# Kernel optimization log

Measured on AMD Instinct MI355X. Metric: run time of the kernel, lower is better.

## Reference

```python
import jax, jax.numpy as jnp
from jax import lax
import numpy as np

EPS = 1e-5
NEG_SLOPE = 0.2

# 4D conv via lax.conv_general_dilated (supports arbitrary spatial rank)
_DN = ('NCABXY', 'OIABXY', 'NCABXY')  # N,C + 4 spatial dims

def conv4d(x, w):
    # x: (N, Cin, S1, S2, H, W); w: (Cout, Cin, 3, 3, 3, 3); padding=1, stride=1
    return lax.conv_general_dilated(
        x, w,
        window_strides=(1, 1, 1, 1),
        padding=[(1, 1)] * 4,
        dimension_numbers=_DN,
    )

def instance_norm4d(x):
    # normalize per (n, c) over all 4 spatial dims; no affine (PyTorch default)
    mean = jnp.mean(x, axis=(2, 3, 4, 5), keepdims=True)
    var = jnp.var(x, axis=(2, 3, 4, 5), keepdims=True)
    return (x - mean) * lax.rsqrt(var + EPS)

def leaky_relu(x):
    return jnp.where(x >= 0, x, NEG_SLOPE * x)

def setup_inputs() -> dict:
    key = jax.random.key(0)
    k0, k1, k2 = jax.random.split(key, 3)
    image = jax.random.normal(k0, (1, 16, 8, 16, 64, 64), dtype=jnp.float32)
    # He-ish init scale for kernel 3^4
    w1 = jax.random.normal(k1, (32, 16, 3, 3, 3, 3), dtype=jnp.float32) * 0.03
    w2 = jax.random.normal(k2, (32, 32, 3, 3, 3, 3), dtype=jnp.float32) * 0.02
    return {"image": image, "w1": w1, "w2": w2}

def reference(image, w1, w2):
    x = leaky_relu(instance_norm4d(conv4d(image, w1)))
    x = leaky_relu(instance_norm4d(conv4d(x, w2)))
    return x
```

## Files before the change

### kernel.cpp

```cpp
#include <hip/hip_runtime.h>

#define D1 8
#define D2 16
#define HH 64
#define WW 64
#define SPATIAL (D1*D2*HH*WW)
#define EPS 1e-5f
#define NEG 0.2f

typedef unsigned short u16;
typedef __attribute__((ext_vector_type(8))) short s16x8;
typedef __attribute__((ext_vector_type(8))) unsigned short u16x8;
typedef __attribute__((ext_vector_type(4))) unsigned short u16x4;
typedef __attribute__((ext_vector_type(4))) float f32x4;

__device__ __forceinline__ u16 f2bf(float f) {
    unsigned int u = __builtin_bit_cast(unsigned int, f);
    return (u16)((u + 0x7FFFu + ((u >> 16) & 1u)) >> 16);
}
__device__ __forceinline__ float bf2f(u16 u) {
    unsigned int v = ((unsigned int)u) << 16;
    return __builtin_bit_cast(float, v);
}
__device__ __forceinline__ float leaky(float x) {
    return x >= 0.f ? x : NEG * x;
}

__device__ __forceinline__ void decode_block(int flat, int& a, int& b, int& h0) {
    int xcd  = flat & 7;
    int slot = flat >> 3;
    int ht   = slot & 7;
    int b0   = (slot >> 3) & 1;
    a        = (slot >> 4) & 7;
    b        = xcd * 2 + b0;
    h0       = ht * 8;
}

__global__ __launch_bounds__(256) void wtrans1(const float* __restrict__ w,
                                               u16* __restrict__ o) {
    int i = blockIdx.x * 256 + threadIdx.x;
    if (i >= 55296) return;
    int k    = i & 31;
    int co   = (i >> 5) & 31;
    int grp  = (i >> 10) & 1;
    int rest = i >> 11;
    int dh   = rest % 3;
    int p    = rest / 3;
    int da = p / 3, db = p % 3;
    float v = 0.f;
    if (grp == 0) {
        int dw = k >> 4, ci = k & 15;
        v = w[((((co * 16 + ci) * 3 + da) * 3 + db) * 3 + dh) * 3 + dw];
    } else if (k < 16) {
        v = w[((((co * 16 + k) * 3 + da) * 3 + db) * 3 + dh) * 3 + 2];
    }
    o[i] = f2bf(v);
}

__global__ __launch_bounds__(256) void wtrans2(const float* __restrict__ w,
                                               u16* __restrict__ o) {
    int i = blockIdx.x * 256 + threadIdx.x;
    if (i >= 82944) return;
    int ci = i & 31;
    int co = (i >> 5) & 31;
    int t  = (i >> 10) % 9;
    int p  = (i >> 10) / 9;
    int da = p / 3, db = p % 3, dh = t / 3, dw = t % 3;
    o[i] = f2bf(w[((((co * 32 + ci) * 3 + da) * 3 + db) * 3 + dh) * 3 + dw]);
}

__global__ __launch_bounds__(256) void imgtrans(const float* __restrict__ img,
                                                u16* __restrict__ o) {
    int p = blockIdx.x * 256 + threadIdx.x;
    u16 r[16];
    #pragma unroll
    for (int c = 0; c < 16; ++c)
        r[c] = f2bf(img[(size_t)c * SPATIAL + p]);
    u16x8 lo, hi;
    #pragma unroll
    for (int j = 0; j < 8; ++j) { lo[j] = r[j]; hi[j] = r[8 + j]; }
    u16x8* dst = (u16x8*)(o + (size_t)p * 16);
    dst[0] = lo;
    dst[1] = hi;
}

__global__ __launch_bounds__(256, 2)
void conv1_mfma(const u16* __restrict__ xT, const u16* __restrict__ w1t,
                u16* __restrict__ y1, float* __restrict__ st1)
{
    __shared__ __align__(16) u16 lds[660 * 24];
    __shared__ float sred[64];

    const int tid = threadIdx.x;
    int a, b, h0;
    decode_block(blockIdx.x, a, b, h0);
    const int lane = tid & 63;
    const int wv   = tid >> 6;
    const int kq   = lane >> 4;
    const int m    = lane & 15;
    const int wseg = wv << 4;

    unsigned pm = 0;
    #pragma unroll
    for (int p = 0; p < 9; ++p) {
        int ap = a + p / 3 - 1, bp = b + p % 3 - 1;
        if (ap >= 0 && ap < D1 && bp >= 0 && bp < D2) pm |= 1u << p;
    }

    const int p0 = tid >> 1, g = tid & 1;
    unsigned vmask = 0;
    int goff[6];
    #pragma unroll
    for (int k = 0; k < 6; ++k) {
        int pos = p0 + 128 * k;
        int row = pos / 66, col = pos - row * 66;
        int h = h0 - 1 + row, w = col - 1;
        bool v = (pos < 660) && col >= 1 && col <= 64 && h >= 0 && h < HH;
        goff[k] = v ? (h * WW + w) * 16 + g * 8 : 0;
        vmask |= (unsigned)v << k;
    }
    const int lbase = p0 * 24 + g * 8;

    for (int e = tid; e < 660; e += 256) {
        int row = e / 66, col = e - row * 66;
        int h = h0 - 1 + row;
        if (col == 0 || col == 65 || h < 0 || h >= HH) {
            u16x8 z = (u16x8)0;
            *(u16x8*)&lds[e * 24]     = z;
            *(u16x8*)&lds[e * 24 + 8] = z;
        }
    }

    f32x4 acc[8][2];
    #pragma unroll
    for (int i = 0; i < 8; ++i)
        #pragma unroll
        for (int nt = 0; nt < 2; ++nt)
            acc[i][nt] = (f32x4)0.f;

    int p = 0;
    while (!((pm >> p) & 1)) ++p;

    u16x8 pf[6];
    {
        int ap = a + p / 3 - 1, bp = b + p % 3 - 1;
        const u16* src = xT + (size_t)(ap * D2 + bp) * (HH * WW * 16);
        #pragma unroll
        for (int k = 0; k < 6; ++k)
            if ((vmask >> k) & 1) pf[k] = *(const u16x8*)(src + goff[k]);
    }

    while (p < 9) {
        int pn = p + 1;
        while (pn < 9 && !((pm >> pn) & 1)) ++pn;

        #pragma unroll
        for (int k = 0; k < 6; ++k)
            if ((vmask >> k) & 1) *(u16x8*)&lds[lbase + k * 3072] = pf[k];
        __syncthreads();

        if (pn < 9) {
            int ap = a + pn / 3 - 1, bp = b + pn % 3 - 1;
            const u16* src = xT + (size_t)(ap * D2 + bp) * (HH * WW * 16);
            #pragma unroll
            for (int k = 0; k < 6; ++k)
                if ((vmask >> k) & 1) pf[k] = *(const u16x8*)(src + goff[k]);
        }

        const u16* wbase = w1t + p * 6144;
        #pragma unroll
        for (int grp = 0; grp < 2; ++grp) {
            s16x8 bf[3][2];
            #pragma unroll
            for (int dh = 0; dh < 3; ++dh) {
                const u16* wb = wbase + (dh * 2 + grp) * 1024;
                bf[dh][0] = *(const s16x8*)(wb + m * 32 + kq * 8);
                bf[dh][1] = *(const s16x8*)(wb + (m + 16) * 32 + kq * 8);
            }
            const int cshift = (grp == 0) ? (kq >> 1) : 2;
            const int ebase  = (kq & 1) * 8;
            #pragma unroll
            for (int x = 0; x < 10; ++x) {
                int pos = x * 66 + wseg + m + cshift;
                s16x8 af = *(const s16x8*)&lds[pos * 24 + ebase];
                #pragma unroll
                for (int dh = 0; dh < 3; ++dh) {
                    int i = x - dh;
                    if (i >= 0 && i < 8) {
                        acc[i][0] = __builtin_amdgcn_mfma_f32_16x16x32_bf16(af, bf[dh][0], acc[i][0], 0, 0, 0);
                        acc[i][1] = __builtin_amdgcn_mfma_f32_16x16x32_bf16(af, bf[dh][1], acc[i][1], 0, 0, 0);
                    }
                }
            }
        }
        __syncthreads();
        p = pn;
    }

    if (tid < 64) sred[tid] = 0.f;
    __syncthreads();

    float s[2] = {0.f, 0.f}, s2[2] = {0.f, 0.f};
    const size_t plane_out = (size_t)(a * D2 + b) * (HH * WW);
    #pragma unroll
    for (int i = 0; i < 8; ++i) {
        int h  = h0 + i;
        int w0 = wseg + kq * 4;
        #pragma unroll
        for (int nt = 0; nt < 2; ++nt) {
            int co = m + nt * 16;
            #pragma unroll
            for (int reg = 0; reg < 4; ++reg) {
                float v = acc[i][nt][reg];
                s[nt]  += v;
                s2[nt] += v * v;
                y1[(plane_out + h * WW + (w0 + reg)) * 32 + co] = f2bf(v);
            }
        }
    }
    #pragma unroll
    for (int nt = 0; nt < 2; ++nt) {
        s[nt]  += __shfl_xor(s[nt], 16);  s[nt]  += __shfl_xor(s[nt], 32);
        s2[nt] += __shfl_xor(s2[nt], 16); s2[nt] += __shfl_xor(s2[nt], 32);
    }
    if (kq == 0) {
        atomicAdd(&sred[m * 2],            s[0]);
        atomicAdd(&sred[m * 2 + 1],        s2[0]);
        atomicAdd(&sred[(m + 16) * 2],     s[1]);
        atomicAdd(&sred[(m + 16) * 2 + 1], s2[1]);
    }
    __syncthreads();
    if (tid < 64) atomicAdd(&st1[tid], sred[tid]);
}

__global__ __launch_bounds__(256)
void norm1_kernel(u16* __restrict__ y1, const float* __restrict__ st1)
{
    const int tid = threadIdx.x;
    const int q   = tid & 3;
    const float invN = 1.f / (float)SPATIAL;
    float mean[8], scl[8];
    #pragma unroll
    for (int j = 0; j < 8; ++j) {
        int ci  = q * 8 + j;
        float mu = st1[ci * 2] * invN;
        float va = st1[ci * 2 + 1] * invN - mu * mu;
        mean[j] = mu;
        scl[j]  = rsqrtf(va + EPS);
    }
    #pragma unroll
    for (int j4 = 0; j4 < 4; ++j4) {
        size_t gidx = (size_t)blockIdx.x * 1024 + j4 * 256 + tid;
        u16x8* ptr = (u16x8*)(y1 + gidx * 8);
        u16x8 v = *ptr;
        u16x8 o;
        #pragma unroll
        for (int j = 0; j < 8; ++j)
            o[j] = f2bf(leaky((bf2f(v[j]) - mean[j]) * scl[j]));
        *ptr = o;
    }
}

__global__ __launch_bounds__(256, 2)
void conv2_mfma(const u16* __restrict__ y1, const u16* __restrict__ w2t,
                u16* __restrict__ y2, float* __restrict__ st2)
{
    __shared__ __align__(16) u16 lds[660 * 40];
    __shared__ float sred[64];

    const int tid = threadIdx.x;
    int a, b, h0;
    decode_block(blockIdx.x, a, b, h0);
    const int lane = tid & 63;
    const int wv   = tid >> 6;
    const int kq   = lane >> 4;
    const int m    = lane & 15;
    const int wseg = wv << 4;

    unsigned pm = 0;
    #pragma unroll
    for (int p = 0; p < 9; ++p) {
        int ap = a + p / 3 - 1, bp = b + p % 3 - 1;
        if (ap >= 0 && ap < D1 && bp >= 0 && bp < D2) pm |= 1u << p;
    }

    const int p0 = tid >> 2, q = tid & 3;
    unsigned vmask = 0;
    int goff[11];
    #pragma unroll
    for (int k = 0; k < 11; ++k) {
        int pos = p0 + 64 * k;
        int row = pos / 66, col = pos - row * 66;
        int h = h0 - 1 + row, w = col - 1;
        bool v = (pos < 660) && col >= 1 && col <= 64 && h >= 0 && h < HH;
        goff[k] = v ? (h * WW + w) * 32 + q * 8 : 0;
        vmask |= (unsigned)v << k;
    }
    const int lbase = p0 * 40 + q * 8;

    for (int e = tid; e < 660; e += 256) {
        int row = e / 66, col = e - row * 66;
        int h = h0 - 1 + row;
        if (col == 0 || col == 65 || h < 0 || h >= HH) {
            u16x8 z = (u16x8)0;
            #pragma unroll
            for (int gg = 0; gg < 4; ++gg)
                *(u16x8*)&lds[e * 40 + gg * 8] = z;
        }
    }

    f32x4 acc[8][2];
    #pragma unroll
    for (int i = 0; i < 8; ++i)
        #pragma unroll
        for (int nt = 0; nt < 2; ++nt)
            acc[i][nt] = (f32x4)0.f;

    int p = 0;
    while (!((pm >> p) & 1)) ++p;

    u16x8 pf[11];
    {
        int ap = a + p / 3 - 1, bp = b + p % 3 - 1;
        const u16* src = y1 + (size_t)(ap * D2 + bp) * (HH * WW * 32);
        #pragma unroll
        for (int k = 0; k < 11; ++k)
            if ((vmask >> k) & 1) pf[k] = *(const u16x8*)(src + goff[k]);
    }

    while (p < 9) {
        int pn = p + 1;
        while (pn < 9 && !((pm >> pn) & 1)) ++pn;

        #pragma unroll
        for (int k = 0; k < 11; ++k)
            if ((vmask >> k) & 1) *(u16x8*)&lds[lbase + k * 2560] = pf[k];
        __syncthreads();

        if (pn < 9) {
            int ap = a + pn / 3 - 1, bp = b + pn % 3 - 1;
            const u16* src = y1 + (size_t)(ap * D2 + bp) * (HH * WW * 32);
            #pragma unroll
            for (int k = 0; k < 11; ++k)
                if ((vmask >> k) & 1) pf[k] = *(const u16x8*)(src + goff[k]);
        }

        const u16* wbase = w2t + p * 9216;
        #pragma unroll
        for (int dw = 0; dw < 3; ++dw) {
            s16x8 bf[3][2];
            #pragma unroll
            for (int dh = 0; dh < 3; ++dh) {
                const u16* wb = wbase + (dh * 3 + dw) * 1024;
                bf[dh][0] = *(const s16x8*)(wb + m * 32 + kq * 8);
                bf[dh][1] = *(const s16x8*)(wb + (m + 16) * 32 + kq * 8);
            }
            #pragma unroll
            for (int x = 0; x < 10; ++x) {
                int pos = x * 66 + wseg + dw + m;
                s16x8 af = *(const s16x8*)&lds[pos * 40 + kq * 8];
                #pragma unroll
                for (int dh = 0; dh < 3; ++dh) {
                    int i = x - dh;
                    if (i >= 0 && i < 8) {
                        acc[i][0] = __builtin_amdgcn_mfma_f32_16x16x32_bf16(af, bf[dh][0], acc[i][0], 0, 0, 0);
                        acc[i][1] = __builtin_amdgcn_mfma_f32_16x16x32_bf16(af, bf[dh][1], acc[i][1], 0, 0, 0);
                    }
                }
            }
        }
        __syncthreads();
        p = pn;
    }

    if (tid < 64) sred[tid] = 0.f;
    __syncthreads();

    float s[2] = {0.f, 0.f}, s2[2] = {0.f, 0.f};
    #pragma unroll
    for (int i = 0; i < 8; ++i) {
        int h  = h0 + i;
        int w0 = wseg + kq * 4;
        #pragma unroll
        for (int nt = 0; nt < 2; ++nt) {
            int co = m + nt * 16;
            u16x4 pk;
            #pragma unroll
            for (int reg = 0; reg < 4; ++reg) {
                float v = acc[i][nt][reg];
                s[nt]  += v;
                s2[nt] += v * v;
                pk[reg] = f2bf(v);
            }
            size_t off = ((size_t)(co * D1 + a) * D2 + b) * (HH * WW) + h * WW + w0;
            *(u16x4*)(y2 + off) = pk;
        }
    }
    #pragma unroll
    for (int nt = 0; nt < 2; ++nt) {
        s[nt]  += __shfl_xor(s[nt], 16);  s[nt]  += __shfl_xor(s[nt], 32);
        s2[nt] += __shfl_xor(s2[nt], 16); s2[nt] += __shfl_xor(s2[nt], 32);
    }
    if (kq == 0) {
        atomicAdd(&sred[m * 2],            s[0]);
        atomicAdd(&sred[m * 2 + 1],        s2[0]);
        atomicAdd(&sred[(m + 16) * 2],     s[1]);
        atomicAdd(&sred[(m + 16) * 2 + 1], s2[1]);
    }
    __syncthreads();
    if (tid < 64) atomicAdd(&st2[tid], sred[tid]);
}

__global__ __launch_bounds__(256)
void norm2_kernel(const u16* __restrict__ y2, const float* __restrict__ st2,
                  float* __restrict__ out)
{
    size_t i4 = (size_t)blockIdx.x * 256 + threadIdx.x;
    int c = (int)(i4 >> 17);
    const float invN = 1.f / (float)SPATIAL;
    float mu = st2[c * 2] * invN;
    float va = st2[c * 2 + 1] * invN - mu * mu;
    float sc = rsqrtf(va + EPS);
    u16x4 v = *(const u16x4*)(y2 + i4 * 4);
    float4 o;
    o.x = leaky((bf2f(v[0]) - mu) * sc);
    o.y = leaky((bf2f(v[1]) - mu) * sc);
    o.z = leaky((bf2f(v[2]) - mu) * sc);
    o.w = leaky((bf2f(v[3]) - mu) * sc);
    *(float4*)(out + i4 * 4) = o;
}

extern "C" void kernel_launch(void* const* d_in, const int* in_sizes, int n_in,
                              void* d_out, int out_size, void* d_ws, size_t ws_size,
                              hipStream_t stream)
{
    const float* image = (const float*)d_in[0];
    const float* w1    = (const float*)d_in[1];
    const float* w2    = (const float*)d_in[2];
    float* out = (float*)d_out;

    u16*   imgT = (u16*)d_ws;
    u16*   y1   = (u16*)((char*)d_ws + 33554432);
    u16*   y2   = imgT;
    float* st   = (float*)((char*)d_ws + 67108864);
    float* st1  = st;
    float* st2  = st + 64;

    u16* w1t = (u16*)((char*)d_out + 66832384);
    u16* w2t = (u16*)((char*)d_out + 66942976);

    hipMemsetAsync(st, 0, 512, stream);
    wtrans1<<<216, 256, 0, stream>>>(w1, w1t);
    wtrans2<<<324, 256, 0, stream>>>(w2, w2t);
    imgtrans<<<2048, 256, 0, stream>>>(image, imgT);

    conv1_mfma<<<1024, 256, 0, stream>>>(imgT, w1t, y1, st1);
    norm1_kernel<<<2048, 256, 0, stream>>>(y1, st1);
    conv2_mfma<<<1024, 256, 0, stream>>>(y1, w2t, y2, st2);
    norm2_kernel<<<16384, 256, 0, stream>>>(y2, st2, out);
}
```

Before: 277.2 us.

## Merge prep kernels, spread next-plane prefetch loads, raise conv occupancy

Folds the memset, both weight transposes and the image transpose into a single prep kernel, saving three launches. Inside both conv kernels, the global prefetch of the next plane is split into chunks placed after each group of MFMA work instead of one burst, which should overlap loads with compute and lower peak register pressure. Launch bounds for both conv kernels go from 2 to 3 blocks per SM, which may force register spilling but allows more occupancy to hide latency.

```diff
diff --git a/kernel.cpp b/kernel.cpp
--- a/kernel.cpp
+++ b/kernel.cpp
@@ -36,55 +36,58 @@
     h0       = ht * 8;
 }
 
-__global__ __launch_bounds__(256) void wtrans1(const float* __restrict__ w,
-                                               u16* __restrict__ o) {
-    int i = blockIdx.x * 256 + threadIdx.x;
-    if (i >= 55296) return;
-    int k    = i & 31;
-    int co   = (i >> 5) & 31;
-    int grp  = (i >> 10) & 1;
-    int rest = i >> 11;
-    int dh   = rest % 3;
-    int p    = rest / 3;
-    int da = p / 3, db = p % 3;
-    float v = 0.f;
-    if (grp == 0) {
-        int dw = k >> 4, ci = k & 15;
-        v = w[((((co * 16 + ci) * 3 + da) * 3 + db) * 3 + dh) * 3 + dw];
-    } else if (k < 16) {
-        v = w[((((co * 16 + k) * 3 + da) * 3 + db) * 3 + dh) * 3 + 2];
-    }
-    o[i] = f2bf(v);
-}
-
-__global__ __launch_bounds__(256) void wtrans2(const float* __restrict__ w,
-                                               u16* __restrict__ o) {
-    int i = blockIdx.x * 256 + threadIdx.x;
-    if (i >= 82944) return;
-    int ci = i & 31;
-    int co = (i >> 5) & 31;
-    int t  = (i >> 10) % 9;
-    int p  = (i >> 10) / 9;
-    int da = p / 3, db = p % 3, dh = t / 3, dw = t % 3;
-    o[i] = f2bf(w[((((co * 32 + ci) * 3 + da) * 3 + db) * 3 + dh) * 3 + dw]);
-}
-
-__global__ __launch_bounds__(256) void imgtrans(const float* __restrict__ img,
-                                                u16* __restrict__ o) {
-    int p = blockIdx.x * 256 + threadIdx.x;
-    u16 r[16];
-    #pragma unroll
-    for (int c = 0; c < 16; ++c)
-        r[c] = f2bf(img[(size_t)c * SPATIAL + p]);
-    u16x8 lo, hi;
-    #pragma unroll
-    for (int j = 0; j < 8; ++j) { lo[j] = r[j]; hi[j] = r[8 + j]; }
-    u16x8* dst = (u16x8*)(o + (size_t)p * 16);
-    dst[0] = lo;
-    dst[1] = hi;
-}
-
-__global__ __launch_bounds__(256, 2)
+__global__ __launch_bounds__(256)
+void prep(const float* __restrict__ img, const float* __restrict__ w1,
+          const float* __restrict__ w2, u16* __restrict__ imgT,
+          u16* __restrict__ w1t, u16* __restrict__ w2t, float* __restrict__ st)
+{
+    const int bid = blockIdx.x;
+    const int tid = threadIdx.x;
+    if (bid < 2048) {
+        int p = bid * 256 + tid;
+        u16 r[16];
+        #pragma unroll
+        for (int c = 0; c < 16; ++c)
+            r[c] = f2bf(img[(size_t)c * SPATIAL + p]);
+        u16x8 lo, hi;
+        #pragma unroll
+        for (int j = 0; j < 8; ++j) { lo[j] = r[j]; hi[j] = r[8 + j]; }
+        u16x8* dst = (u16x8*)(imgT + (size_t)p * 16);
+        dst[0] = lo;
+        dst[1] = hi;
+    } else if (bid < 2264) {
+        int i = (bid - 2048) * 256 + tid;
+        if (i >= 55296) return;
+        int k    = i & 31;
+        int co   = (i >> 5) & 31;
+        int grp  = (i >> 10) & 1;
+        int rest = i >> 11;
+        int dh   = rest % 3;
+        int p    = rest / 3;
+        int da = p / 3, db = p % 3;
+        float v = 0.f;
+        if (grp == 0) {
+            int dw = k >> 4, ci = k & 15;
+            v = w1[((((co * 16 + ci) * 3 + da) * 3 + db) * 3 + dh) * 3 + dw];
+        } else if (k < 16) {
+            v = w1[((((co * 16 + k) * 3 + da) * 3 + db) * 3 + dh) * 3 + 2];
+        }
+        w1t[i] = f2bf(v);
+    } else if (bid < 2588) {
+        int i = (bid - 2264) * 256 + tid;
+        if (i >= 82944) return;
+        int ci = i & 31;
+        int co = (i >> 5) & 31;
+        int t  = (i >> 10) % 9;
+        int p  = (i >> 10) / 9;
+        int da = p / 3, db = p % 3, dh = t / 3, dw = t % 3;
+        w2t[i] = f2bf(w2[((((co * 32 + ci) * 3 + da) * 3 + db) * 3 + dh) * 3 + dw]);
+    } else {
+        if (tid < 128) st[tid] = 0.f;
+    }
+}
+
+__global__ __launch_bounds__(256, 3)
 void conv1_mfma(const u16* __restrict__ xT, const u16* __restrict__ w1t,
                 u16* __restrict__ y1, float* __restrict__ st1)
 {
@@ -159,13 +162,10 @@
             if ((vmask >> k) & 1) *(u16x8*)&lds[lbase + k * 3072] = pf[k];
         __syncthreads();
 
-        if (pn < 9) {
-            int ap = a + pn / 3 - 1, bp = b + pn % 3 - 1;
-            const u16* src = xT + (size_t)(ap * D2 + bp) * (HH * WW * 16);
-            #pragma unroll
-            for (int k = 0; k < 6; ++k)
-                if ((vmask >> k) & 1) pf[k] = *(const u16x8*)(src + goff[k]);
-        }
+        const u16* srcn = nullptr;
+        if (pn < 9)
+            srcn = xT + (size_t)((a + pn / 3 - 1) * D2 + (b + pn % 3 - 1))
+                      * (HH * WW * 16);
 
         const u16* wbase = w1t + p * 6144;
         #pragma unroll
@@ -192,6 +192,11 @@
                     }
                 }
             }
+            if (pn < 9) {
+                #pragma unroll
+                for (int k = grp * 3; k < grp * 3 + 3; ++k)
+                    if ((vmask >> k) & 1) pf[k] = *(const u16x8*)(srcn + goff[k]);
+            }
         }
         __syncthreads();
         p = pn;
@@ -261,7 +266,7 @@
     }
 }
 
-__global__ __launch_bounds__(256, 2)
+__global__ __launch_bounds__(256, 3)
 void conv2_mfma(const u16* __restrict__ y1, const u16* __restrict__ w2t,
                 u16* __restrict__ y2, float* __restrict__ st2)
 {
@@ -337,13 +342,10 @@
             if ((vmask >> k) & 1) *(u16x8*)&lds[lbase + k * 2560] = pf[k];
         __syncthreads();
 
-        if (pn < 9) {
-            int ap = a + pn / 3 - 1, bp = b + pn % 3 - 1;
-            const u16* src = y1 + (size_t)(ap * D2 + bp) * (HH * WW * 32);
-            #pragma unroll
-            for (int k = 0; k < 11; ++k)
-                if ((vmask >> k) & 1) pf[k] = *(const u16x8*)(src + goff[k]);
-        }
+        const u16* srcn = nullptr;
+        if (pn < 9)
+            srcn = y1 + (size_t)((a + pn / 3 - 1) * D2 + (b + pn % 3 - 1))
+                      * (HH * WW * 32);
 
         const u16* wbase = w2t + p * 9216;
         #pragma unroll
@@ -367,6 +369,13 @@
                         acc[i][1] = __builtin_amdgcn_mfma_f32_16x16x32_bf16(af, bf[dh][1], acc[i][1], 0, 0, 0);
                     }
                 }
+            }
+            if (pn < 9) {
+                const int k0 = dw * 4;
+                const int k1 = (dw == 2) ? 11 : (k0 + 4);
+                #pragma unroll
+                for (int k = k0; k < k1; ++k)
+                    if ((vmask >> k) & 1) pf[k] = *(const u16x8*)(srcn + goff[k]);
             }
         }
         __syncthreads();
@@ -449,10 +458,7 @@
     u16* w1t = (u16*)((char*)d_out + 66832384);
     u16* w2t = (u16*)((char*)d_out + 66942976);
 
-    hipMemsetAsync(st, 0, 512, stream);
-    wtrans1<<<216, 256, 0, stream>>>(w1, w1t);
-    wtrans2<<<324, 256, 0, stream>>>(w2, w2t);
-    imgtrans<<<2048, 256, 0, stream>>>(image, imgT);
+    prep<<<2589, 256, 0, stream>>>(image, w1, w2, imgT, w1t, w2t, st);
 
     conv1_mfma<<<1024, 256, 0, stream>>>(imgT, w1t, y1, st1);
     norm1_kernel<<<2048, 256, 0, stream>>>(y1, st1);
```

Measured after the change: 265.9 us. -4.1%, faster.
